# Kernel optimization log

Measured on AMD Instinct MI355X. Metric: run time of the kernel, lower is better.

The kernel has to match this reference:

```python
import jax, jax.numpy as jnp
import numpy as np

NUM_HEADS = 8
NUM_GROUPS = 32  # min(C//4, 32) for C=512
EPS = 1e-6       # flax GroupNorm default


def setup_inputs() -> dict:
    key = jax.random.key(0)
    ks = jax.random.split(key, 3)
    B, H, W, D, C = 2, 16, 16, 16, 512
    x = jax.random.normal(ks[0], (B, H, W, D, C), dtype=jnp.float32)
    w_qkv = jax.random.normal(ks[1], (C, 3 * C), dtype=jnp.float32) / np.sqrt(C)
    w_proj = jax.random.normal(ks[2], (C, C), dtype=jnp.float32) / np.sqrt(C)
    return {
        "x": x,
        "gn_scale": jnp.ones((C,), jnp.float32),
        "gn_bias": jnp.zeros((C,), jnp.float32),
        "w_qkv": w_qkv,
        "b_qkv": jnp.zeros((3 * C,), jnp.float32),
        "w_proj": w_proj,
        "b_proj": jnp.zeros((C,), jnp.float32),
    }


def group_norm(x, scale, bias):
    # x: [B, S, C]; normalize within each of NUM_GROUPS channel groups over (S, group-channels)
    B, S, C = x.shape
    xg = x.reshape(B, S, NUM_GROUPS, C // NUM_GROUPS)
    mean = jnp.mean(xg, axis=(1, 3), keepdims=True)
    var = jnp.var(xg, axis=(1, 3), keepdims=True)
    xn = (xg - mean) * jax.lax.rsqrt(var + EPS)
    return xn.reshape(B, S, C) * scale + bias


def reference(x, gn_scale, gn_bias, w_qkv, b_qkv, w_proj, b_proj):
    B, H, W, D, C = x.shape
    S = H * W * D
    hd = C // NUM_HEADS
    xf = x.reshape(B, S, C)
    q_in = group_norm(xf, gn_scale, gn_bias)
    # 1x1x1 conv == per-position dense
    qkv = q_in @ w_qkv + b_qkv                      # [B, S, 3C]
    qkv = qkv.reshape(B, S, NUM_HEADS, 3 * hd)
    q, k, v = jnp.split(qkv, 3, axis=-1)            # each [B, S, nh, hd]
    scale = 1.0 / jnp.sqrt(jnp.asarray(hd, x.dtype))
    logits = jnp.einsum('btnh,bfnh->bnft', k, q * scale)  # [B, nh, S, S]
    weights = jax.nn.softmax(logits, axis=-1)
    h = jnp.einsum('bnft,btnh->bfnh', weights, v)   # [B, S, nh, hd]
    h = h.reshape(B, S, C) @ w_proj + b_proj
    return h.reshape(x.shape) + x
```

## Files before the change

kernel.cpp:

```cpp
#include <hip/hip_runtime.h>

typedef __attribute__((ext_vector_type(8))) short short8;
typedef __attribute__((ext_vector_type(4))) float f32x4;
typedef __attribute__((ext_vector_type(16))) float f32x16;

#define S_LEN 4096
#define C_DIM 512
#define NH 8
#define HD 64
#define NG 32
#define GS 16
#define LOG2E 1.44269504088896340736f

__device__ __forceinline__ unsigned short f2bf(float f) {
  union { float f; unsigned int u; } v; v.f = f;
  unsigned int r = v.u + 0x7fffu + ((v.u >> 16) & 1u);
  return (unsigned short)(r >> 16);
}

__device__ __forceinline__ float bf2f(unsigned short s) {
  union { unsigned u; float f; } v; v.u = (unsigned)s << 16;
  return v.f;
}

__device__ __forceinline__ float fexp2(float x) {
  float r;
  asm("v_exp_f32 %0, %1" : "=v"(r) : "v"(x));
  return r;
}

__device__ __forceinline__ unsigned pk_bf16(float a, float b) {
  unsigned r;
  asm("v_cvt_pk_bf16_f32 %0, %1, %2" : "=v"(r) : "v"(a), "v"(b));
  return r;
}

__device__ __forceinline__ void pl_swapf(float& a, float& b) {
  asm("v_permlane32_swap_b32 %0, %1" : "+v"(a), "+v"(b));
}

__device__ __forceinline__ void gload_lds16(const void* g, void* l) {
  __builtin_amdgcn_global_load_lds((const __attribute__((address_space(1))) void*)g,
                                   (__attribute__((address_space(3))) void*)l, 16, 0, 0);
}

__global__ __launch_bounds__(256) void prep_kernel(const float* __restrict__ x,
                                                   float* __restrict__ partials,
                                                   const float* __restrict__ w_qkv,
                                                   unsigned short* __restrict__ wqkvT,
                                                   const float* __restrict__ w_proj,
                                                   unsigned short* __restrict__ wprojT) {
  __shared__ float tile[32][33];
  __shared__ float r1[4], r2[4];
  int bid = blockIdx.x;
  if (bid < 256) {
    int bg = bid >> 2, chunk = bid & 3;
    int b = bg >> 5, g = bg & 31;
    const float* xp = x + (size_t)b * S_LEN * C_DIM + g * GS;
    float s1 = 0.f, s2 = 0.f;
    for (int i = threadIdx.x; i < 1024 * 4; i += 256) {
      int s = chunk * 1024 + (i >> 2), c4 = i & 3;
      float4 v = *(const float4*)&xp[(size_t)s * C_DIM + c4 * 4];
      s1 += v.x + v.y + v.z + v.w;
      s2 += v.x * v.x + v.y * v.y + v.z * v.z + v.w * v.w;
    }
    for (int off = 1; off < 64; off <<= 1) {
      s1 += __shfl_xor(s1, off);
      s2 += __shfl_xor(s2, off);
    }
    int w = threadIdx.x >> 6;
    if ((threadIdx.x & 63) == 0) { r1[w] = s1; r2[w] = s2; }
    __syncthreads();
    if (threadIdx.x == 0) {
      partials[bg * 8 + chunk * 2]     = r1[0] + r1[1] + r1[2] + r1[3];
      partials[bg * 8 + chunk * 2 + 1] = r2[0] + r2[1] + r2[2] + r2[3];
    }
    return;
  }
  const float* src; unsigned short* dst; int K, N, n0, k0;
  if (bid < 1024) {
    int t = bid - 256;  src = w_qkv;  dst = wqkvT;  K = 512; N = 1536;
    n0 = (t % 48) * 32; k0 = (t / 48) * 32;
  } else {
    int t = bid - 1024; src = w_proj; dst = wprojT; K = 512; N = 512;
    n0 = (t % 16) * 32; k0 = (t / 16) * 32;
  }
  int c = threadIdx.x & 31, r0 = threadIdx.x >> 5;
  for (int i = 0; i < 4; ++i) {
    int r = r0 + i * 8;
    tile[r][c] = src[(size_t)(k0 + r) * N + n0 + c];
  }
  __syncthreads();
  for (int i = 0; i < 4; ++i) {
    int r = r0 + i * 8;
    dst[(size_t)(n0 + r) * K + k0 + c] = f2bf(tile[c][r]);
  }
}

__global__ __launch_bounds__(256) void gn_apply_kernel(const float* __restrict__ x,
                                                       const float* __restrict__ partials,
                                                       const float* __restrict__ scale,
                                                       const float* __restrict__ bias,
                                                       unsigned short* __restrict__ out) {
  int idx = blockIdx.x * 256 + threadIdx.x;
  int e = idx * 4;
  int c = e & (C_DIM - 1);
  int bs = e >> 9;
  int b = bs >> 12;
  int grp = b * NG + (c >> 4);
  float s1 = partials[grp * 8] + partials[grp * 8 + 2] + partials[grp * 8 + 4] + partials[grp * 8 + 6];
  float s2 = partials[grp * 8 + 1] + partials[grp * 8 + 3] + partials[grp * 8 + 5] + partials[grp * 8 + 7];
  const float invN = 1.0f / (float)(S_LEN * GS);
  float mean = s1 * invN;
  float var = s2 * invN - mean * mean;
  float rstd = rsqrtf(var + 1e-6f);
  float4 v = *(const float4*)&x[e];
  ushort4 o;
  o.x = f2bf((v.x - mean) * rstd * scale[c]     + bias[c]);
  o.y = f2bf((v.y - mean) * rstd * scale[c + 1] + bias[c + 1]);
  o.z = f2bf((v.z - mean) * rstd * scale[c + 2] + bias[c + 2]);
  o.w = f2bf((v.w - mean) * rstd * scale[c + 3] + bias[c + 3]);
  *(ushort4*)&out[e] = o;
}

__global__ __launch_bounds__(256) void gemm_qkv_kernel(const unsigned short* __restrict__ A,
                                                       const unsigned short* __restrict__ Bt,
                                                       const float* __restrict__ bias,
                                                       unsigned short* __restrict__ qh,
                                                       unsigned short* __restrict__ kh,
                                                       unsigned short* __restrict__ vh) {
  __shared__ unsigned char Alds[16384];
  __shared__ unsigned char Blds[16384];
  int tid = threadIdx.x, lane = tid & 63, w = tid >> 6;
  int li = lane & 15, g = lane >> 4;
  int wr = (w >> 1) * 64, wc = (w & 1) * 64;
  int m0 = blockIdx.y * 128, n0 = blockIdx.x * 128;

  int srow = tid >> 3;
  int colS = (tid & 7) * 16;
  int sc   = colS ^ ((srow & 7) << 4);
  const char* aSrc = (const char*)A + (size_t)(m0 + srow) * 1024 + sc;
  const char* bSrc = (const char*)Bt + (size_t)(n0 + srow) * 1024 + sc;

  f32x4 acc[4][4];
  for (int i = 0; i < 4; ++i)
    for (int j = 0; j < 4; ++j) acc[i][j] = (f32x4){0.f, 0.f, 0.f, 0.f};

  for (int k0 = 0; k0 < 512; k0 += 64) {
#pragma unroll
    for (int r = 0; r < 4; ++r) {
      gload_lds16(aSrc + (size_t)r * 32 * 1024 + k0 * 2, &Alds[r * 4096 + tid * 16]);
      gload_lds16(bSrc + (size_t)r * 32 * 1024 + k0 * 2, &Blds[r * 4096 + tid * 16]);
    }
    asm volatile("s_waitcnt vmcnt(0)" ::: "memory");
    __builtin_amdgcn_s_barrier();

#pragma unroll
    for (int ks = 0; ks < 2; ++ks) {
      short8 af[4], bfm[4];
#pragma unroll
      for (int mi = 0; mi < 4; ++mi) {
        int row = wr + mi * 16 + li;
        af[mi] = *(const short8*)&Alds[row * 128 + ((ks * 64 + g * 16) ^ ((row & 7) << 4))];
      }
#pragma unroll
      for (int ni = 0; ni < 4; ++ni) {
        int row = wc + ni * 16 + li;
        bfm[ni] = *(const short8*)&Blds[row * 128 + ((ks * 64 + g * 16) ^ ((row & 7) << 4))];
      }
#pragma unroll
      for (int mi = 0; mi < 4; ++mi)
#pragma unroll
        for (int ni = 0; ni < 4; ++ni)
          acc[mi][ni] = __builtin_amdgcn_mfma_f32_16x16x32_bf16(af[mi], bfm[ni], acc[mi][ni], 0, 0, 0);
    }
    __syncthreads();
  }

  for (int ni = 0; ni < 4; ++ni) {
    int n = n0 + wc + ni * 16 + li;
    float bn = bias[n];
    int head = n / 192;
    int rem = n - head * 192;
    int part = rem >> 6;
    int h = rem & 63;
    if (part == 2) {
      for (int mi = 0; mi < 4; ++mi) {
        int m = m0 + wr + mi * 16 + g * 4;
        int b = m >> 12, s = m & 4095;
        size_t idx = ((size_t)(b * NH + head) * HD + h) * S_LEN + s;
        ushort4 val;
        val.x = f2bf(acc[mi][ni][0] + bn);
        val.y = f2bf(acc[mi][ni][1] + bn);
        val.z = f2bf(acc[mi][ni][2] + bn);
        val.w = f2bf(acc[mi][ni][3] + bn);
        *(ushort4*)&vh[idx] = val;
      }
    } else {
      unsigned short* dst = part == 0 ? qh : kh;
      float mul = part == 0 ? 0.125f * LOG2E : 1.0f;
      for (int mi = 0; mi < 4; ++mi)
        for (int j = 0; j < 4; ++j) {
          int m = m0 + wr + mi * 16 + g * 4 + j;
          int b = m >> 12, s = m & 4095;
          dst[((size_t)(b * NH + head) * S_LEN + s) * HD + h] = f2bf((acc[mi][ni][j] + bn) * mul);
        }
    }
  }
}

__global__ __launch_bounds__(256) void gemm_plain_kernel(const unsigned short* __restrict__ A,
                                                         const unsigned short* __restrict__ Bt,
                                                         const float* __restrict__ bias,
                                                         const float* __restrict__ resid,
                                                         float* __restrict__ outf) {
  __shared__ unsigned char Alds[16384];
  __shared__ unsigned char Blds[16384];
  int tid = threadIdx.x, lane = tid & 63, w = tid >> 6;
  int li = lane & 15, g = lane >> 4;
  int wr = (w >> 1) * 64, wc = (w & 1) * 64;
  int m0 = blockIdx.y * 128, n0 = blockIdx.x * 128;

  int srow = tid >> 3;
  int colS = (tid & 7) * 16;
  int sc   = colS ^ ((srow & 7) << 4);
  const char* aSrc = (const char*)A + (size_t)(m0 + srow) * 1024 + sc;
  const char* bSrc = (const char*)Bt + (size_t)(n0 + srow) * 1024 + sc;

  f32x4 acc[4][4];
  for (int i = 0; i < 4; ++i)
    for (int j = 0; j < 4; ++j) acc[i][j] = (f32x4){0.f, 0.f, 0.f, 0.f};

  for (int k0 = 0; k0 < 512; k0 += 64) {
#pragma unroll
    for (int r = 0; r < 4; ++r) {
      gload_lds16(aSrc + (size_t)r * 32 * 1024 + k0 * 2, &Alds[r * 4096 + tid * 16]);
      gload_lds16(bSrc + (size_t)r * 32 * 1024 + k0 * 2, &Blds[r * 4096 + tid * 16]);
    }
    asm volatile("s_waitcnt vmcnt(0)" ::: "memory");
    __builtin_amdgcn_s_barrier();
#pragma unroll
    for (int ks = 0; ks < 2; ++ks) {
      short8 af[4], bfm[4];
#pragma unroll
      for (int mi = 0; mi < 4; ++mi) {
        int row = wr + mi * 16 + li;
        af[mi] = *(const short8*)&Alds[row * 128 + ((ks * 64 + g * 16) ^ ((row & 7) << 4))];
      }
#pragma unroll
      for (int ni = 0; ni < 4; ++ni) {
        int row = wc + ni * 16 + li;
        bfm[ni] = *(const short8*)&Blds[row * 128 + ((ks * 64 + g * 16) ^ ((row & 7) << 4))];
      }
#pragma unroll
      for (int mi = 0; mi < 4; ++mi)
#pragma unroll
        for (int ni = 0; ni < 4; ++ni)
          acc[mi][ni] = __builtin_amdgcn_mfma_f32_16x16x32_bf16(af[mi], bfm[ni], acc[mi][ni], 0, 0, 0);
    }
    __syncthreads();
  }

  for (int ni = 0; ni < 4; ++ni) {
    int n = n0 + wc + ni * 16 + li;
    float bn = bias[n];
    for (int mi = 0; mi < 4; ++mi)
      for (int j = 0; j < 4; ++j) {
        int m = m0 + wr + mi * 16 + g * 4 + j;
        size_t off = (size_t)m * C_DIM + n;
        outf[off] = acc[mi][ni][j] + bn + resid[off];
      }
  }
}

__global__ __launch_bounds__(256) void gemm_proj_kernel(const unsigned short* __restrict__ opart,
                                                        const float* __restrict__ lpart,
                                                        const unsigned short* __restrict__ Bt,
                                                        const float* __restrict__ bias,
                                                        const float* __restrict__ resid,
                                                        float* __restrict__ outf) {
  __shared__ unsigned char Alds[16384];
  __shared__ unsigned char Blds[16384];
  __shared__ float linv[8][128];
  int tid = threadIdx.x, lane = tid & 63, w = tid >> 6;
  int li = lane & 15, g = lane >> 4;
  int wr = (w >> 1) * 64, wc = (w & 1) * 64;
  int m0 = blockIdx.y * 128, n0 = blockIdx.x * 128;
  int b_ = m0 >> 12;
  int s0 = m0 & 4095;

  int srow = tid >> 3;
  int colS = (tid & 7) * 16;
  int sc   = colS ^ ((srow & 7) << 4);
  const char* bSrc = (const char*)Bt + (size_t)(n0 + srow) * 1024 + sc;

#pragma unroll
  for (int i = 0; i < 4; ++i) {
    int e = tid + i * 256;
    int hd_ = e >> 7, r = e & 127;
    size_t rowA = (size_t)((b_ * NH + hd_) * 2) * S_LEN + s0 + r;
    linv[hd_][r] = 1.0f / (lpart[rowA] + lpart[rowA + S_LEN]);
  }
  __syncthreads();

  int tr = tid >> 1, hf2 = tid & 1;
  size_t rowBase = ((size_t)(b_ * NH) * 2) * S_LEN + s0 + tr;

  f32x4 acc[4][4];
  for (int i = 0; i < 4; ++i)
    for (int j = 0; j < 4; ++j) acc[i][j] = (f32x4){0.f, 0.f, 0.f, 0.f};

  for (int k0 = 0; k0 < 512; k0 += 64) {
    int head = k0 >> 6;
#pragma unroll
    for (int r = 0; r < 4; ++r)
      gload_lds16(bSrc + (size_t)r * 32 * 1024 + k0 * 2, &Blds[r * 4096 + tid * 16]);

    size_t rowA = rowBase + (size_t)head * 2 * S_LEN;
    const unsigned short* pA0 = opart + rowA * 64 + hf2 * 32;
    const unsigned short* pA1 = opart + (rowA + S_LEN) * 64 + hf2 * 32;
    float inv = linv[head][tr];
#pragma unroll
    for (int q = 0; q < 4; ++q) {
      short8 xx = *(const short8*)&pA0[q * 8];
      short8 yy = *(const short8*)&pA1[q * 8];
      union { unsigned u[4]; short8 v; } d;
#pragma unroll
      for (int p = 0; p < 4; ++p) {
        float f0 = (bf2f((unsigned short)xx[2 * p])     + bf2f((unsigned short)yy[2 * p]))     * inv;
        float f1 = (bf2f((unsigned short)xx[2 * p + 1]) + bf2f((unsigned short)yy[2 * p + 1])) * inv;
        d.u[p] = pk_bf16(f0, f1);
      }
      int cc = hf2 * 64 + q * 16;
      *(short8*)&Alds[tr * 128 + (cc ^ ((tr & 7) << 4))] = d.v;
    }
    __syncthreads();

#pragma unroll
    for (int ks = 0; ks < 2; ++ks) {
      short8 af[4], bfm[4];
#pragma unroll
      for (int mi = 0; mi < 4; ++mi) {
        int row = wr + mi * 16 + li;
        af[mi] = *(const short8*)&Alds[row * 128 + ((ks * 64 + g * 16) ^ ((row & 7) << 4))];
      }
#pragma unroll
      for (int ni = 0; ni < 4; ++ni) {
        int row = wc + ni * 16 + li;
        bfm[ni] = *(const short8*)&Blds[row * 128 + ((ks * 64 + g * 16) ^ ((row & 7) << 4))];
      }
#pragma unroll
      for (int mi = 0; mi < 4; ++mi)
#pragma unroll
        for (int ni = 0; ni < 4; ++ni)
          acc[mi][ni] = __builtin_amdgcn_mfma_f32_16x16x32_bf16(af[mi], bfm[ni], acc[mi][ni], 0, 0, 0);
    }
    __syncthreads();
  }

  for (int ni = 0; ni < 4; ++ni) {
    int n = n0 + wc + ni * 16 + li;
    float bn = bias[n];
    for (int mi = 0; mi < 4; ++mi)
      for (int j = 0; j < 4; ++j) {
        int m = m0 + wr + mi * 16 + g * 4 + j;
        size_t off = (size_t)m * C_DIM + n;
        outf[off] = acc[mi][ni][j] + bn + resid[off];
      }
  }
}

template <int SPLIT>
__global__ __launch_bounds__(256, 4) void attn_kernel(const unsigned short* __restrict__ qh,
                                                      const unsigned short* __restrict__ kh,
                                                      const unsigned short* __restrict__ vt,
                                                      unsigned short* __restrict__ ob,
                                                      unsigned short* __restrict__ opart,
                                                      float* __restrict__ lpart) {
  __shared__ unsigned char Kt[3 * 4096];
  __shared__ unsigned char Vt[3 * 4096];
  int bn = blockIdx.y;
  int half = SPLIT > 1 ? blockIdx.z : 0;
  int tid = threadIdx.x, lane = tid & 63, wv = tid >> 6;
  int r32 = lane & 31, hi_ = lane >> 5;
  int q0 = blockIdx.x * 128 + wv * 32;
  const int NT = S_LEN / 32 / SPLIT;
  const unsigned short* qp = qh + (size_t)bn * S_LEN * HD;
  const char* kp = (const char*)(kh + (size_t)bn * S_LEN * HD);
  const char* vp = (const char*)(vt + (size_t)bn * HD * S_LEN);

  int srow  = wv * 8 + (lane >> 3);
  int scolS = (lane & 7) * 16;
  int sc    = scolS ^ ((srow & 7) << 4);
  const char* kSrc = kp + (size_t)srow * 128 + sc + (size_t)half * (S_LEN / SPLIT) * 128;
  int vh_ = srow + ((sc >> 6) << 5);
  const char* vSrc = vp + (size_t)vh_ * (S_LEN * 2) + (sc & 63) + (size_t)half * (S_LEN / SPLIT) * 2;

  short8 qf[4];
#pragma unroll
  for (int ks = 0; ks < 4; ++ks)
    qf[ks] = *(const short8*)&qp[(size_t)(q0 + r32) * HD + ks * 16 + hi_ * 8];

  f32x16 o0, o1, z16;
#pragma unroll
  for (int i = 0; i < 16; ++i) { o0[i] = 0.f; o1[i] = 0.f; z16[i] = 0.f; }
  float lsum = 0.f;

  int kRow = (r32 & 3) + 4 * (r32 >> 3) + 8 * (r32 >> 4) + 8 * ((r32 >> 2) & 1);
  int swzk = (kRow & 7) << 4;
  int swzr = (r32 & 7) << 4;
  int sBase = wv * 1024;

  gload_lds16(kSrc, &Kt[sBase]);
  gload_lds16(vSrc, &Vt[sBase]);
  gload_lds16(kSrc + 32 * 128, &Kt[4096 + sBase]);
  gload_lds16(vSrc + 32 * 2,   &Vt[4096 + sBase]);
  asm volatile("s_waitcnt vmcnt(2)" ::: "memory");
  __builtin_amdgcn_s_barrier();

  int curO = 0, nxtO = 4096, nnO = 8192;
  for (int it = 0; it < NT; ++it) {
    bool more = (it + 2 < NT);
    if (more) {
      size_t t0n = (size_t)(it + 2) * 32;
      gload_lds16(kSrc + t0n * 128, &Kt[nnO + sBase]);
      gload_lds16(vSrc + t0n * 2,   &Vt[nnO + sBase]);
    }

    const unsigned char* Kr = &Kt[curO + kRow * 128];
    const unsigned char* Vr = &Vt[curO + r32 * 128];
    short8 kf[4], vf[4];
#pragma unroll
    for (int ks = 0; ks < 4; ++ks)
      kf[ks] = *(const short8*)&Kr[(ks * 32 + hi_ * 16) ^ swzk];
#pragma unroll
    for (int kk = 0; kk < 2; ++kk)
#pragma unroll
      for (int hf = 0; hf < 2; ++hf)
        vf[kk * 2 + hf] = *(const short8*)&Vr[(hf * 64 + kk * 32 + hi_ * 16) ^ swzr];

    f32x16 s = __builtin_amdgcn_mfma_f32_32x32x16_bf16(kf[0], qf[0], z16, 0, 0, 0);
#pragma unroll
    for (int ks = 1; ks < 4; ++ks)
      s = __builtin_amdgcn_mfma_f32_32x32x16_bf16(kf[ks], qf[ks], s, 0, 0, 0);

#pragma unroll
    for (int i = 0; i < 16; ++i) s[i] = fexp2(s[i]);

    float t0 = (s[0] + s[1]) + (s[2] + s[3]);
    float t1 = (s[4] + s[5]) + (s[6] + s[7]);
    float t2 = (s[8] + s[9]) + (s[10] + s[11]);
    float t3 = (s[12] + s[13]) + (s[14] + s[15]);
    lsum += (t0 + t1) + (t2 + t3);

    union { unsigned u[4]; short8 v; } F0, F1;
    F0.u[0] = pk_bf16(s[0], s[1]);   F0.u[1] = pk_bf16(s[2], s[3]);
    F0.u[2] = pk_bf16(s[4], s[5]);   F0.u[3] = pk_bf16(s[6], s[7]);
    F1.u[0] = pk_bf16(s[8], s[9]);   F1.u[1] = pk_bf16(s[10], s[11]);
    F1.u[2] = pk_bf16(s[12], s[13]); F1.u[3] = pk_bf16(s[14], s[15]);

    o0 = __builtin_amdgcn_mfma_f32_32x32x16_bf16(vf[0], F0.v, o0, 0, 0, 0);
    o1 = __builtin_amdgcn_mfma_f32_32x32x16_bf16(vf[1], F0.v, o1, 0, 0, 0);
    o0 = __builtin_amdgcn_mfma_f32_32x32x16_bf16(vf[2], F1.v, o0, 0, 0, 0);
    o1 = __builtin_amdgcn_mfma_f32_32x32x16_bf16(vf[3], F1.v, o1, 0, 0, 0);

    if (more) asm volatile("s_waitcnt vmcnt(2)" ::: "memory");
    else      asm volatile("s_waitcnt vmcnt(0)" ::: "memory");
    __builtin_amdgcn_s_barrier();
    int t = curO; curO = nxtO; nxtO = nnO; nnO = t;
  }

  { float c2 = lsum; pl_swapf(lsum, c2); lsum += c2; }

  if (SPLIT == 1) {
    float inv = 1.0f / lsum;
    int b = bn >> 3, n = bn & 7;
    size_t base = ((size_t)(b * S_LEN + q0 + r32)) * C_DIM + n * HD;
#pragma unroll
    for (int r = 0; r < 16; ++r) {
      int hrow = (r & 3) + 8 * (r >> 2) + 4 * hi_;
      ob[base + hrow]      = f2bf(o0[r] * inv);
      ob[base + 32 + hrow] = f2bf(o1[r] * inv);
    }
  } else {
    size_t row = (size_t)(bn * SPLIT + half) * S_LEN + q0 + r32;
    unsigned short* pp = opart + row * 64;
#pragma unroll
    for (int i = 0; i < 8; ++i) {
      int r = 2 * i;
      int hrow = (r & 3) + 8 * (r >> 2) + 4 * hi_;
      *(unsigned*)&pp[hrow]      = pk_bf16(o0[r], o0[r + 1]);
      *(unsigned*)&pp[32 + hrow] = pk_bf16(o1[r], o1[r + 1]);
    }
    if (!hi_) lpart[row] = lsum;
  }
}

extern "C" void kernel_launch(void* const* d_in, const int* in_sizes, int n_in,
                              void* d_out, int out_size, void* d_ws, size_t ws_size,
                              hipStream_t stream) {
  const float* x        = (const float*)d_in[0];
  const float* gn_scale = (const float*)d_in[1];
  const float* gn_bias  = (const float*)d_in[2];
  const float* w_qkv    = (const float*)d_in[3];
  const float* b_qkv    = (const float*)d_in[4];
  const float* w_proj   = (const float*)d_in[5];
  const float* b_proj   = (const float*)d_in[6];
  float* out = (float*)d_out;

  char* ws = (char*)d_ws;
  unsigned short* q_in   = (unsigned short*)(ws);
  unsigned short* wqkvT  = (unsigned short*)(ws + 8388608);
  unsigned short* wprojT = (unsigned short*)(ws + 9961472);
  unsigned short* qhb    = (unsigned short*)(ws + 10485760);
  unsigned short* khb    = (unsigned short*)(ws + 18874368);
  unsigned short* vtb    = (unsigned short*)(ws + 27262976);
  unsigned short* ahb    = (unsigned short*)(ws + 35651584);
  float* partials        = (float*)(ws + 44040192);
  float* lpart           = (float*)(ws + 44042240);
  unsigned short* opart  = (unsigned short*)(ws + 45090816);
  const size_t NEED2 = 45090816ull + (size_t)16 * 2 * S_LEN * 64 * 2;

  prep_kernel<<<1280, 256, 0, stream>>>(x, partials, w_qkv, wqkvT, w_proj, wprojT);
  gn_apply_kernel<<<4096, 256, 0, stream>>>(x, partials, gn_scale, gn_bias, q_in);
  gemm_qkv_kernel<<<dim3(12, 64), 256, 0, stream>>>(q_in, wqkvT, b_qkv, qhb, khb, vtb);
  if (ws_size >= NEED2) {
    attn_kernel<2><<<dim3(32, 16, 2), 256, 0, stream>>>(qhb, khb, vtb, nullptr, opart, lpart);
    gemm_proj_kernel<<<dim3(4, 64), 256, 0, stream>>>(opart, lpart, wprojT, b_proj, x, out);
  } else {
    attn_kernel<1><<<dim3(32, 16, 1), 256, 0, stream>>>(qhb, khb, vtb, ahb, nullptr, nullptr);
    gemm_plain_kernel<<<dim3(4, 64), 256, 0, stream>>>(ahb, wprojT, b_proj, x, out);
  }
}
```

Baseline: 146.1 us.

## Software-pipeline attention loop so QK of next tile overlaps softmax-PV

Restructures the attention inner loop into a two-stage software pipeline. The QK^T MFMAs for tile t+1 are issued before the exp, row-sum and PV work for tile t, and the loop is unrolled by two. LDS staging grows from a 3-slot to a 4-slot ring so one tile can be computed on while two more are in flight. The aim is to hide the latency of the exp/pack stage behind matrix ops. In exchange it raises register pressure (two live S tiles) and shared memory use, which could reduce occupancy under the 4-blocks launch bound.

```diff
diff --git a/kernel.cpp b/kernel.cpp
--- a/kernel.cpp
+++ b/kernel.cpp
@@ -377,8 +377,8 @@
                                                       unsigned short* __restrict__ ob,
                                                       unsigned short* __restrict__ opart,
                                                       float* __restrict__ lpart) {
-  __shared__ unsigned char Kt[3 * 4096];
-  __shared__ unsigned char Vt[3 * 4096];
+  __shared__ unsigned char Kt[4 * 4096];
+  __shared__ unsigned char Vt[4 * 4096];
   int bn = blockIdx.y;
   int half = SPLIT > 1 ? blockIdx.z : 0;
   int tid = threadIdx.x, lane = tid & 63, wv = tid >> 6;
@@ -411,63 +411,69 @@
   int swzr = (r32 & 7) << 4;
   int sBase = wv * 1024;
 
-  gload_lds16(kSrc, &Kt[sBase]);
-  gload_lds16(vSrc, &Vt[sBase]);
-  gload_lds16(kSrc + 32 * 128, &Kt[4096 + sBase]);
-  gload_lds16(vSrc + 32 * 2,   &Vt[4096 + sBase]);
-  asm volatile("s_waitcnt vmcnt(2)" ::: "memory");
-  __builtin_amdgcn_s_barrier();
-
-  int curO = 0, nxtO = 4096, nnO = 8192;
-  for (int it = 0; it < NT; ++it) {
-    bool more = (it + 2 < NT);
-    if (more) {
-      size_t t0n = (size_t)(it + 2) * 32;
-      gload_lds16(kSrc + t0n * 128, &Kt[nnO + sBase]);
-      gload_lds16(vSrc + t0n * 2,   &Vt[nnO + sBase]);
-    }
-
-    const unsigned char* Kr = &Kt[curO + kRow * 128];
-    const unsigned char* Vr = &Vt[curO + r32 * 128];
-    short8 kf[4], vf[4];
-#pragma unroll
-    for (int ks = 0; ks < 4; ++ks)
-      kf[ks] = *(const short8*)&Kr[(ks * 32 + hi_ * 16) ^ swzk];
+  auto stage = [&](int t) {
+    int slot = (t & 3) * 4096;
+    gload_lds16(kSrc + (size_t)t * 32 * 128, &Kt[slot + sBase]);
+    gload_lds16(vSrc + (size_t)t * 32 * 2,   &Vt[slot + sBase]);
+  };
+  auto qk = [&](int t) {
+    const unsigned char* Kr = &Kt[(t & 3) * 4096 + kRow * 128];
+    short8 kf0 = *(const short8*)&Kr[(0 * 32 + hi_ * 16) ^ swzk];
+    short8 kf1 = *(const short8*)&Kr[(1 * 32 + hi_ * 16) ^ swzk];
+    short8 kf2 = *(const short8*)&Kr[(2 * 32 + hi_ * 16) ^ swzk];
+    short8 kf3 = *(const short8*)&Kr[(3 * 32 + hi_ * 16) ^ swzk];
+    f32x16 s = __builtin_amdgcn_mfma_f32_32x32x16_bf16(kf0, qf[0], z16, 0, 0, 0);
+    s = __builtin_amdgcn_mfma_f32_32x32x16_bf16(kf1, qf[1], s, 0, 0, 0);
+    s = __builtin_amdgcn_mfma_f32_32x32x16_bf16(kf2, qf[2], s, 0, 0, 0);
+    s = __builtin_amdgcn_mfma_f32_32x32x16_bf16(kf3, qf[3], s, 0, 0, 0);
+    return s;
+  };
+  auto smpv = [&](f32x16& s, int t) {
+    const unsigned char* Vr = &Vt[(t & 3) * 4096 + r32 * 128];
+    short8 vf[4];
 #pragma unroll
     for (int kk = 0; kk < 2; ++kk)
 #pragma unroll
       for (int hf = 0; hf < 2; ++hf)
         vf[kk * 2 + hf] = *(const short8*)&Vr[(hf * 64 + kk * 32 + hi_ * 16) ^ swzr];
-
-    f32x16 s = __builtin_amdgcn_mfma_f32_32x32x16_bf16(kf[0], qf[0], z16, 0, 0, 0);
-#pragma unroll
-    for (int ks = 1; ks < 4; ++ks)
-      s = __builtin_amdgcn_mfma_f32_32x32x16_bf16(kf[ks], qf[ks], s, 0, 0, 0);
-
 #pragma unroll
     for (int i = 0; i < 16; ++i) s[i] = fexp2(s[i]);
-
     float t0 = (s[0] + s[1]) + (s[2] + s[3]);
     float t1 = (s[4] + s[5]) + (s[6] + s[7]);
     float t2 = (s[8] + s[9]) + (s[10] + s[11]);
     float t3 = (s[12] + s[13]) + (s[14] + s[15]);
     lsum += (t0 + t1) + (t2 + t3);
-
     union { unsigned u[4]; short8 v; } F0, F1;
     F0.u[0] = pk_bf16(s[0], s[1]);   F0.u[1] = pk_bf16(s[2], s[3]);
     F0.u[2] = pk_bf16(s[4], s[5]);   F0.u[3] = pk_bf16(s[6], s[7]);
     F1.u[0] = pk_bf16(s[8], s[9]);   F1.u[1] = pk_bf16(s[10], s[11]);
     F1.u[2] = pk_bf16(s[12], s[13]); F1.u[3] = pk_bf16(s[14], s[15]);
-
     o0 = __builtin_amdgcn_mfma_f32_32x32x16_bf16(vf[0], F0.v, o0, 0, 0, 0);
     o1 = __builtin_amdgcn_mfma_f32_32x32x16_bf16(vf[1], F0.v, o1, 0, 0, 0);
     o0 = __builtin_amdgcn_mfma_f32_32x32x16_bf16(vf[2], F1.v, o0, 0, 0, 0);
     o1 = __builtin_amdgcn_mfma_f32_32x32x16_bf16(vf[3], F1.v, o1, 0, 0, 0);
-
-    if (more) asm volatile("s_waitcnt vmcnt(2)" ::: "memory");
-    else      asm volatile("s_waitcnt vmcnt(0)" ::: "memory");
+  };
+
+  stage(0); stage(1); stage(2);
+  asm volatile("s_waitcnt vmcnt(2)" ::: "memory");
+  __builtin_amdgcn_s_barrier();
+  f32x16 sA = qk(0);
+  f32x16 sB;
+
+  for (int it = 0; it < NT; it += 2) {
+    if (it + 3 < NT) stage(it + 3);
+    sB = qk(it + 1);
+    smpv(sA, it);
+    if (it + 3 < NT) asm volatile("s_waitcnt vmcnt(2)" ::: "memory");
+    else             asm volatile("s_waitcnt vmcnt(0)" ::: "memory");
     __builtin_amdgcn_s_barrier();
-    int t = curO; curO = nxtO; nxtO = nnO; nnO = t;
+
+    if (it + 4 < NT) stage(it + 4);
+    if (it + 2 < NT) sA = qk(it + 2);
+    smpv(sB, it + 1);
+    if (it + 4 < NT) asm volatile("s_waitcnt vmcnt(2)" ::: "memory");
+    else             asm volatile("s_waitcnt vmcnt(0)" ::: "memory");
+    __builtin_amdgcn_s_barrier();
   }
 
   { float c2 = lsum; pl_swapf(lsum, c2); lsum += c2; }
```

Result: no change. 147.0 us, median of 2 (+0.6%).
